# Performance work log

Measured on AMD Instinct MI355X. Metric: run time of the kernel, lower is better.

The kernel has to match this reference:

```python
import jax, jax.numpy as jnp
import numpy as np

N_EMBD = 1024
N_HEAD = 16
HEAD_SIZE = N_EMBD // N_HEAD  # 64


def setup_inputs() -> dict:
    key = jax.random.key(0)
    k1, k2, k3, k4 = jax.random.split(key, 4)
    B, T = 4, 4096
    x = jax.random.normal(k1, (B, T, N_EMBD), dtype=jnp.float32)
    scale = 1.0 / np.sqrt(N_EMBD)
    # Linear(n_embd, head_size, bias=False): store as [C, H] so projection is x @ W
    Wk = jax.random.normal(k2, (N_EMBD, HEAD_SIZE), dtype=jnp.float32) * scale
    Wq = jax.random.normal(k3, (N_EMBD, HEAD_SIZE), dtype=jnp.float32) * scale
    Wv = jax.random.normal(k4, (N_EMBD, HEAD_SIZE), dtype=jnp.float32) * scale
    decay_factor = jnp.array([-0.5], dtype=jnp.float32)
    return {"x": x, "Wk": Wk, "Wq": Wq, "Wv": Wv, "decay_factor": decay_factor}


def reference(x, Wk, Wq, Wv, decay_factor):
    B, T, C = x.shape
    H = Wk.shape[1]
    k = x @ Wk  # [B,T,H]
    q = x @ Wq  # [B,T,H]
    v = x @ Wv  # [B,T,H]
    wei = jnp.einsum('bth,bsh->bts', q, k) * (H ** -0.5)  # [B,T,T]
    idx = jnp.arange(T)
    dist = jnp.minimum(idx[None, :] - idx[:, None], 0)  # j - i, clamped max=0
    ripple_bias = dist.astype(x.dtype) * jnp.abs(decay_factor[0])
    wei = wei + ripple_bias[None, :, :]
    causal = idx[None, :] <= idx[:, None]  # tril mask [T,T]
    wei = jnp.where(causal[None, :, :], wei, -jnp.inf)
    wei = jax.nn.softmax(wei, axis=-1)
    return jnp.einsum('bts,bsh->bth', wei, v)
```

## Files before the change

kernel.cpp:

```cpp
#include <hip/hip_runtime.h>

typedef short bf16x8 __attribute__((ext_vector_type(8)));
typedef float f32x4 __attribute__((ext_vector_type(4)));

#define TT 4096
#define CC 1024
#define HH 64
#define MTOT 16384

static __device__ __forceinline__ unsigned short f2bf(float f) {
  unsigned int u = __float_as_uint(f);
  unsigned int r = (u + 0x7FFFu + ((u >> 16) & 1u)) >> 16;
  return (unsigned short)r;
}

static __device__ __forceinline__ unsigned int pack_bf2(float lo, float hi) {
  unsigned int ul = __float_as_uint(lo) + 0x8000u;
  unsigned int uh = __float_as_uint(hi) + 0x8000u;
  return __builtin_amdgcn_perm(uh, ul, 0x07060302u);
}

typedef const __attribute__((address_space(1))) void gvoid;
typedef __attribute__((address_space(3))) void svoid;
static __device__ __forceinline__ void gll16(const void* g, void* l) {
  __builtin_amdgcn_global_load_lds((gvoid*)g, (svoid*)l, 16, 0, 0);
}

#define WAITVM(N) asm volatile("s_waitcnt vmcnt(" #N ")" ::: "memory")

__global__ void prep_wt(const float* __restrict__ Wk, const float* __restrict__ Wq,
                        const float* __restrict__ Wv, unsigned short* __restrict__ Wt) {
  int r = blockIdx.x;
  const float* src = (r < 64) ? Wk : ((r < 128) ? Wq : Wv);
  int c = r & 63;
  for (int kk = threadIdx.x; kk < CC; kk += blockDim.x)
    Wt[(size_t)r * CC + kk] = f2bf(src[(size_t)kk * HH + c]);
}

__global__ __launch_bounds__(512, 2) void proj_kernel(
    const float* __restrict__ x, const unsigned short* __restrict__ Wt,
    unsigned short* __restrict__ kb, unsigned short* __restrict__ qb,
    unsigned short* __restrict__ vt) {
  extern __shared__ __align__(16) char smem[];
  float* Xl = (float*)smem;
  unsigned short* Bl = (unsigned short*)(smem + 32768);

  const int tid = threadIdx.x;
  const int lane = tid & 63;
  const int w = tid >> 6;
  const int r = lane & 15, g = lane >> 4;
  const int rowgrp = w >> 1;
  const int colbase = (w & 1) * 96;
  const int m0 = blockIdx.x * 64;

  const float* xsrcs[2];
#pragma unroll
  for (int j = 0; j < 2; ++j) {
    int c = j * 512 + tid;
    int row = c >> 4, s = c & 15;
    xsrcs[j] = x + (size_t)(m0 + row) * CC + (((s & 8) | ((s & 7) ^ (row & 7))) * 4);
  }
  const unsigned short* bsrcs[3];
#pragma unroll
  for (int j = 0; j < 3; ++j) {
    int cb = j * 512 + tid;
    int row = cb >> 3, s = cb & 7;
    bsrcs[j] = Wt + (size_t)row * CC + ((s ^ (row & 7)) * 8);
  }

  f32x4 acc[6];
#pragma unroll
  for (int n = 0; n < 6; ++n) { f32x4 z = {0.f, 0.f, 0.f, 0.f}; acc[n] = z; }

  auto stage = [&](int t, int buf) {
    float* xb = Xl + buf * 4096;
    unsigned short* bb = Bl + buf * 12288;
#pragma unroll
    for (int j = 0; j < 2; ++j)
      gll16(xsrcs[j] + t * 64, xb + (j * 512 + w * 64) * 4);
#pragma unroll
    for (int j = 0; j < 3; ++j)
      gll16(bsrcs[j] + t * 64, bb + (size_t)(j * 512 + w * 64) * 8);
  };

  const int rr = rowgrp * 16 + r;
  const int rb = rr * 64;
  const int rx = rr & 7;

  auto body = [&](int buf) {
    const float* xb = Xl + buf * 4096;
    const unsigned short* bb = Bl + buf * 12288;
    bf16x8 bfr[2][6];
#pragma unroll
    for (int ks = 0; ks < 2; ++ks)
#pragma unroll
      for (int n = 0; n < 6; ++n) {
        int col = colbase + 16 * n + r;
        bfr[ks][n] = *(const bf16x8*)&bb[col * 64 + (((ks * 4 + g) ^ (col & 7)) * 8)];
      }
#pragma unroll
    for (int ks = 0; ks < 2; ++ks) {
      int s0 = ks * 8 + 2 * g;
      f32x4 v0 = *(const f32x4*)&xb[rb + (((s0 & 8) | ((s0 & 7) ^ rx)) * 4)];
      f32x4 v1 = *(const f32x4*)&xb[rb + ((((s0 + 1) & 8) | (((s0 + 1) & 7) ^ rx)) * 4)];
      union { bf16x8 v; unsigned int u[4]; } af;
      af.u[0] = pack_bf2(v0.x, v0.y);
      af.u[1] = pack_bf2(v0.z, v0.w);
      af.u[2] = pack_bf2(v1.x, v1.y);
      af.u[3] = pack_bf2(v1.z, v1.w);
#pragma unroll
      for (int n = 0; n < 6; ++n)
        acc[n] = __builtin_amdgcn_mfma_f32_16x16x32_bf16(af.v, bfr[ks][n], acc[n], 0, 0, 0);
    }
  };

  stage(0, 0);
  stage(1, 1);

  for (int t = 0; t < 14; ++t) {
    WAITVM(5);
    __builtin_amdgcn_s_barrier();
    body(t & 1);
    __builtin_amdgcn_s_barrier();
    stage(t + 2, t & 1);
  }
  WAITVM(5); __builtin_amdgcn_s_barrier(); body(0);
  WAITVM(0); __builtin_amdgcn_s_barrier(); body(1);

#pragma unroll
  for (int n = 0; n < 6; ++n) {
#pragma unroll
    for (int i = 0; i < 4; ++i) {
      int row = m0 + rowgrp * 16 + 4 * g + i;
      int col = colbase + 16 * n + r;
      unsigned short h = f2bf(acc[n][i]);
      if (col < 64) {
        kb[(size_t)row * HH + col] = h;
      } else if (col < 128) {
        qb[(size_t)row * HH + (col - 64)] = h;
      } else {
        int dim = col - 128;
        int b = row >> 12;
        int tt = row & (TT - 1);
        vt[(((size_t)b * HH + dim) << 12) + tt] = h;
      }
    }
  }
}

__global__ __launch_bounds__(256, 2) void attn_kernel(
    const unsigned short* __restrict__ qb, const unsigned short* __restrict__ kb,
    const unsigned short* __restrict__ vt, const float* __restrict__ decayp,
    float* __restrict__ out) {
  __shared__ __align__(16) unsigned short Kl[2 * 64 * 64];
  __shared__ __align__(16) unsigned short Vl[2 * 64 * 64];
  __shared__ __align__(16) unsigned short Pl[4][16 * 64];
  __shared__ float Ml[32], Ll[32];
  __shared__ float Ol[32][64];

  const int tid = threadIdx.x;
  const int lane = tid & 63;
  const int w = tid >> 6;
  const int r = lane & 15, g = lane >> 4;
  const int qh = w & 1;
  const int kvg = w >> 1;

  const int batch = blockIdx.x & 3;
  const int qt = blockIdx.x >> 2;
  const int qbase = qt * 32;
  const int qw = qbase + qh * 16;

  const float decay = fabsf(decayp[0]);

  const unsigned short* qbb = qb + (size_t)batch * TT * HH;
  const unsigned short* kbb = kb + (size_t)batch * TT * HH;
  const unsigned short* vbb = vt + (size_t)batch * HH * TT;

  const unsigned short* qp = qbb + (size_t)(qw + r) * HH;
  bf16x8 aq0 = *(const bf16x8*)(qp + 8 * g);
  bf16x8 aq1 = *(const bf16x8*)(qp + 32 + 8 * g);

  int t0 = 0;
  if (decay > 1e-8f) {
    float wf = 60.f / decay;
    if (wf < (float)TT) {
      int W = (int)wf + 1;
      int lo = qbase - W;
      if (lo < 0) lo = 0;
      t0 = lo >> 6;
    }
  }
  const int t1 = (qbase + 31) >> 6;
  const int nsteps = (t1 - t0 + 2) >> 1;

  float m[4], lsum[4];
  f32x4 o[4];
#pragma unroll
  for (int i = 0; i < 4; ++i) {
    m[i] = -1e30f; lsum[i] = 0.f;
    f32x4 z = {0.f, 0.f, 0.f, 0.f}; o[i] = z;
  }

  for (int s = 0; s < nsteps; ++s) {
    const int tA = t0 + 2 * s;
    const int tB = (tA + 1 <= t1) ? tA + 1 : t1;
#pragma unroll
    for (int j = 0; j < 4; ++j) {
      int c = j * 256 + tid;
      int th = c >> 9;
      int cc = c & 511;
      int row = cc >> 3, sl = cc & 7;
      int tile = th ? tB : tA;
      bf16x8 kvv = *(const bf16x8*)(kbb + (size_t)(tile * 64 + row) * HH + ((sl ^ (row & 7)) * 8));
      *(bf16x8*)&Kl[c * 8] = kvv;
      bf16x8 vvv = *(const bf16x8*)(vbb + (size_t)row * TT + tile * 64 + ((sl ^ (row & 7)) * 8));
      *(bf16x8*)&Vl[c * 8] = vvv;
    }
    __syncthreads();

    const int myt = tA + kvg;
    if (myt <= t1) {
      const unsigned short* Kb = &Kl[kvg * 4096];
      const unsigned short* Vb = &Vl[kvg * 4096];
      const int kv0 = myt * 64;

      f32x4 sacc[4];
#pragma unroll
      for (int t = 0; t < 4; ++t) {
        f32x4 z = {0.f, 0.f, 0.f, 0.f}; sacc[t] = z;
        int kvr = 16 * t + r;
        bf16x8 b0 = *(const bf16x8*)&Kb[kvr * 64 + ((g ^ (kvr & 7)) * 8)];
        bf16x8 b1 = *(const bf16x8*)&Kb[kvr * 64 + (((4 + g) ^ (kvr & 7)) * 8)];
        sacc[t] = __builtin_amdgcn_mfma_f32_16x16x32_bf16(aq0, b0, sacc[t], 0, 0, 0);
        sacc[t] = __builtin_amdgcn_mfma_f32_16x16x32_bf16(aq1, b1, sacc[t], 0, 0, 0);
      }

      float p[4][4];
      float rmax[4], rsum[4], al[4];
#pragma unroll
      for (int i = 0; i < 4; ++i) rmax[i] = -1e30f;
#pragma unroll
      for (int t = 0; t < 4; ++t) {
        int kv = kv0 + 16 * t + r;
#pragma unroll
        for (int i = 0; i < 4; ++i) {
          int q = qw + 4 * g + i;
          float sv = sacc[t][i] * 0.125f + decay * (float)(kv - q);
          if (kv > q) sv = -1e30f;
          p[t][i] = sv;
          rmax[i] = fmaxf(rmax[i], sv);
        }
      }
#pragma unroll
      for (int i = 0; i < 4; ++i) {
#pragma unroll
        for (int d = 1; d < 16; d <<= 1)
          rmax[i] = fmaxf(rmax[i], __shfl_xor(rmax[i], d, 64));
        float mn = fmaxf(m[i], rmax[i]);
        al[i] = __expf(m[i] - mn);
        m[i] = mn;
        rsum[i] = 0.f;
      }
#pragma unroll
      for (int t = 0; t < 4; ++t)
#pragma unroll
        for (int i = 0; i < 4; ++i) {
          float e = __expf(p[t][i] - m[i]);
          p[t][i] = e;
          rsum[i] += e;
        }
#pragma unroll
      for (int i = 0; i < 4; ++i) {
#pragma unroll
        for (int d = 1; d < 16; d <<= 1)
          rsum[i] += __shfl_xor(rsum[i], d, 64);
        lsum[i] = lsum[i] * al[i] + rsum[i];
      }
#pragma unroll
      for (int n = 0; n < 4; ++n) {
        o[n][0] *= al[0]; o[n][1] *= al[1]; o[n][2] *= al[2]; o[n][3] *= al[3];
      }

      unsigned short* P = &Pl[w][0];
#pragma unroll
      for (int t = 0; t < 4; ++t) {
#pragma unroll
        for (int i = 0; i < 4; ++i) {
          int row = 4 * g + i;
          int col = 16 * t + r;
          int slot = col >> 3;
          P[row * 64 + ((slot ^ (row & 7)) * 8) + (col & 7)] = f2bf(p[t][i]);
        }
      }
      bf16x8 pa0 = *(const bf16x8*)&P[r * 64 + ((g ^ (r & 7)) * 8)];
      bf16x8 pa1 = *(const bf16x8*)&P[r * 64 + (((4 + g) ^ (r & 7)) * 8)];

#pragma unroll
      for (int n = 0; n < 4; ++n) {
        int dim = 16 * n + r;
        bf16x8 v0 = *(const bf16x8*)&Vb[dim * 64 + ((g ^ (dim & 7)) * 8)];
        bf16x8 v1 = *(const bf16x8*)&Vb[dim * 64 + (((4 + g) ^ (dim & 7)) * 8)];
        o[n] = __builtin_amdgcn_mfma_f32_16x16x32_bf16(pa0, v0, o[n], 0, 0, 0);
        o[n] = __builtin_amdgcn_mfma_f32_16x16x32_bf16(pa1, v1, o[n], 0, 0, 0);
      }
    }
    __syncthreads();
  }

  if (kvg == 1) {
    if (r == 0) {
#pragma unroll
      for (int i = 0; i < 4; ++i) {
        Ml[qh * 16 + 4 * g + i] = m[i];
        Ll[qh * 16 + 4 * g + i] = lsum[i];
      }
    }
#pragma unroll
    for (int n = 0; n < 4; ++n)
#pragma unroll
      for (int i = 0; i < 4; ++i)
        Ol[qh * 16 + 4 * g + i][16 * n + r] = o[n][i];
  }
  __syncthreads();
  if (kvg == 0) {
    float* ob = out + (size_t)batch * TT * HH;
#pragma unroll
    for (int i = 0; i < 4; ++i) {
      int row = qh * 16 + 4 * g + i;
      float m2 = Ml[row], l2 = Ll[row];
      float M = fmaxf(m[i], m2);
      float e1 = __expf(m[i] - M), e2 = __expf(m2 - M);
      float inv = 1.f / (lsum[i] * e1 + l2 * e2);
#pragma unroll
      for (int n = 0; n < 4; ++n) {
        float ov = (o[n][i] * e1 + Ol[row][16 * n + r] * e2) * inv;
        ob[(size_t)(qbase + row) * HH + 16 * n + r] = ov;
      }
    }
  }
}

extern "C" void kernel_launch(void* const* d_in, const int* in_sizes, int n_in,
                              void* d_out, int out_size, void* d_ws, size_t ws_size,
                              hipStream_t stream) {
  const float* x = (const float*)d_in[0];
  const float* Wk = (const float*)d_in[1];
  const float* Wq = (const float*)d_in[2];
  const float* Wv = (const float*)d_in[3];
  const float* decay = (const float*)d_in[4];
  float* out = (float*)d_out;

  unsigned short* kb = (unsigned short*)d_ws;
  unsigned short* qbw = kb + (size_t)MTOT * HH;
  unsigned short* vt = qbw + (size_t)MTOT * HH;
  unsigned short* Wt = vt + (size_t)MTOT * HH;

  prep_wt<<<dim3(192), dim3(256), 0, stream>>>(Wk, Wq, Wv, Wt);
  proj_kernel<<<dim3(256), dim3(512), 80 * 1024, stream>>>(x, Wt, kb, qbw, vt);
  attn_kernel<<<dim3(512), dim3(256), 0, stream>>>(qbw, kb, vt, decay, out);
}
```

Before: 34.52 us.

## Pipeline attention KV loads via async LDS, triple-buffer projection, transpose weights via LDS

Weight prep now transposes 64x64 tiles through shared memory with coalesced vector loads and stores, replacing strided scalar reads. The projection kernel moves from double to triple buffering with deeper vmcnt waits, which needs 120KB of LDS. The attention kernel switches to double-buffered async global-to-LDS loads that overlap with compute. It also swaps MFMA operands so each lane owns one query row, which removes most shuffles and yields coalesced float4 output stores through LDS. The larger LDS footprint may cut occupancy, and the stage/wait counts need careful bookkeeping.

```diff
diff --git a/kernel.cpp b/kernel.cpp
--- a/kernel.cpp
+++ b/kernel.cpp
@@ -30,11 +30,30 @@
 
 __global__ void prep_wt(const float* __restrict__ Wk, const float* __restrict__ Wq,
                         const float* __restrict__ Wv, unsigned short* __restrict__ Wt) {
-  int r = blockIdx.x;
-  const float* src = (r < 64) ? Wk : ((r < 128) ? Wq : Wv);
-  int c = r & 63;
-  for (int kk = threadIdx.x; kk < CC; kk += blockDim.x)
-    Wt[(size_t)r * CC + kk] = f2bf(src[(size_t)kk * HH + c]);
+  __shared__ float T[64][65];
+  const int mat = blockIdx.x >> 4;
+  const int kt = blockIdx.x & 15;
+  const float* src = (mat == 0) ? Wk : ((mat == 1) ? Wq : Wv);
+#pragma unroll
+  for (int i = 0; i < 4; ++i) {
+    int c = i * 256 + threadIdx.x;
+    int row = c >> 4, col = (c & 15) * 4;
+    f32x4 v = *(const f32x4*)&src[(size_t)(kt * 64 + row) * HH + col];
+    T[col + 0][row] = v[0];
+    T[col + 1][row] = v[1];
+    T[col + 2][row] = v[2];
+    T[col + 3][row] = v[3];
+  }
+  __syncthreads();
+#pragma unroll
+  for (int i = 0; i < 2; ++i) {
+    int c2 = i * 256 + threadIdx.x;
+    int row = c2 >> 3, k0 = (c2 & 7) * 8;
+    union { bf16x8 v; unsigned short h[8]; } pk;
+#pragma unroll
+    for (int j = 0; j < 8; ++j) pk.h[j] = f2bf(T[row][k0 + j]);
+    *(bf16x8*)&Wt[(size_t)(mat * 64 + row) * CC + kt * 64 + k0] = pk.v;
+  }
 }
 
 __global__ __launch_bounds__(512, 2) void proj_kernel(
@@ -43,7 +62,7 @@
     unsigned short* __restrict__ vt) {
   extern __shared__ __align__(16) char smem[];
   float* Xl = (float*)smem;
-  unsigned short* Bl = (unsigned short*)(smem + 32768);
+  unsigned short* Bl = (unsigned short*)(smem + 49152);
 
   const int tid = threadIdx.x;
   const int lane = tid & 63;
@@ -116,16 +135,20 @@
 
   stage(0, 0);
   stage(1, 1);
-
-  for (int t = 0; t < 14; ++t) {
-    WAITVM(5);
+  stage(2, 2);
+
+  int buf = 0;
+  for (int t = 0; t < 13; ++t) {
+    WAITVM(10);
     __builtin_amdgcn_s_barrier();
-    body(t & 1);
+    body(buf);
     __builtin_amdgcn_s_barrier();
-    stage(t + 2, t & 1);
-  }
-  WAITVM(5); __builtin_amdgcn_s_barrier(); body(0);
-  WAITVM(0); __builtin_amdgcn_s_barrier(); body(1);
+    stage(t + 3, buf);
+    buf = (buf == 2) ? 0 : buf + 1;
+  }
+  WAITVM(10); __builtin_amdgcn_s_barrier(); body(1);
+  WAITVM(5);  __builtin_amdgcn_s_barrier(); body(2);
+  WAITVM(0);  __builtin_amdgcn_s_barrier(); body(0);
 
 #pragma unroll
   for (int n = 0; n < 6; ++n) {
@@ -152,11 +175,13 @@
     const unsigned short* __restrict__ qb, const unsigned short* __restrict__ kb,
     const unsigned short* __restrict__ vt, const float* __restrict__ decayp,
     float* __restrict__ out) {
-  __shared__ __align__(16) unsigned short Kl[2 * 64 * 64];
-  __shared__ __align__(16) unsigned short Vl[2 * 64 * 64];
-  __shared__ __align__(16) unsigned short Pl[4][16 * 64];
-  __shared__ float Ml[32], Ll[32];
-  __shared__ float Ol[32][64];
+  extern __shared__ __align__(16) char smem[];
+  unsigned short* Kl = (unsigned short*)smem;
+  unsigned short* Vl = Kl + 16384;
+  unsigned short* Pl = Vl + 16384;
+  float* Ol = (float*)(smem + 65536);
+  float* Ml = (float*)(smem + 65536 + 8704);
+  float* Ll = Ml + 32;
 
   const int tid = threadIdx.x;
   const int lane = tid & 63;
@@ -169,6 +194,7 @@
   const int qt = blockIdx.x >> 2;
   const int qbase = qt * 32;
   const int qw = qbase + qh * 16;
+  const int qrow = qw + r;
 
   const float decay = fabsf(decayp[0]);
 
@@ -176,7 +202,7 @@
   const unsigned short* kbb = kb + (size_t)batch * TT * HH;
   const unsigned short* vbb = vt + (size_t)batch * HH * TT;
 
-  const unsigned short* qp = qbb + (size_t)(qw + r) * HH;
+  const unsigned short* qp = qbb + (size_t)qrow * HH;
   bf16x8 aq0 = *(const bf16x8*)(qp + 8 * g);
   bf16x8 aq1 = *(const bf16x8*)(qp + 32 + 8 * g);
 
@@ -193,150 +219,148 @@
   const int t1 = (qbase + 31) >> 6;
   const int nsteps = (t1 - t0 + 2) >> 1;
 
-  float m[4], lsum[4];
+  const unsigned short* ksrc[4];
+  const unsigned short* vsrc[4];
+#pragma unroll
+  for (int j = 0; j < 4; ++j) {
+    int c = j * 256 + tid;
+    int th = c >> 9;
+    int cc = c & 511;
+    int row = cc >> 3, sl = cc & 7;
+    ksrc[j] = kbb + (size_t)((t0 + th) * 64 + row) * HH + ((sl ^ (row & 7)) * 8);
+    vsrc[j] = vbb + (size_t)row * TT + (t0 + th) * 64 + ((sl ^ (row & 7)) * 8);
+  }
+
+  auto stage = [&](int s, int buf) {
+#pragma unroll
+    for (int j = 0; j < 4; ++j) {
+      gll16(ksrc[j] + (size_t)s * 8192, Kl + buf * 8192 + (j * 256 + w * 64) * 8);
+      gll16(vsrc[j] + s * 128, Vl + buf * 8192 + (j * 256 + w * 64) * 8);
+    }
+  };
+
+  float m = -1e30f, lsum = 0.f;
   f32x4 o[4];
 #pragma unroll
-  for (int i = 0; i < 4; ++i) {
-    m[i] = -1e30f; lsum[i] = 0.f;
-    f32x4 z = {0.f, 0.f, 0.f, 0.f}; o[i] = z;
-  }
+  for (int n = 0; n < 4; ++n) { f32x4 z = {0.f, 0.f, 0.f, 0.f}; o[n] = z; }
+
+  stage(0, 0);
 
   for (int s = 0; s < nsteps; ++s) {
-    const int tA = t0 + 2 * s;
-    const int tB = (tA + 1 <= t1) ? tA + 1 : t1;
-#pragma unroll
-    for (int j = 0; j < 4; ++j) {
-      int c = j * 256 + tid;
-      int th = c >> 9;
-      int cc = c & 511;
-      int row = cc >> 3, sl = cc & 7;
-      int tile = th ? tB : tA;
-      bf16x8 kvv = *(const bf16x8*)(kbb + (size_t)(tile * 64 + row) * HH + ((sl ^ (row & 7)) * 8));
-      *(bf16x8*)&Kl[c * 8] = kvv;
-      bf16x8 vvv = *(const bf16x8*)(vbb + (size_t)row * TT + tile * 64 + ((sl ^ (row & 7)) * 8));
-      *(bf16x8*)&Vl[c * 8] = vvv;
-    }
-    __syncthreads();
-
-    const int myt = tA + kvg;
+    if (s + 1 < nsteps) { stage(s + 1, (s + 1) & 1); WAITVM(8); }
+    else { WAITVM(0); }
+    __builtin_amdgcn_s_barrier();
+
+    const int myt = t0 + 2 * s + kvg;
     if (myt <= t1) {
-      const unsigned short* Kb = &Kl[kvg * 4096];
-      const unsigned short* Vb = &Vl[kvg * 4096];
+      const unsigned short* Kb = Kl + (s & 1) * 8192 + kvg * 4096;
+      const unsigned short* Vb = Vl + (s & 1) * 8192 + kvg * 4096;
       const int kv0 = myt * 64;
 
       f32x4 sacc[4];
+      __builtin_amdgcn_s_setprio(1);
 #pragma unroll
       for (int t = 0; t < 4; ++t) {
-        f32x4 z = {0.f, 0.f, 0.f, 0.f}; sacc[t] = z;
+        f32x4 z = {0.f, 0.f, 0.f, 0.f};
         int kvr = 16 * t + r;
         bf16x8 b0 = *(const bf16x8*)&Kb[kvr * 64 + ((g ^ (kvr & 7)) * 8)];
         bf16x8 b1 = *(const bf16x8*)&Kb[kvr * 64 + (((4 + g) ^ (kvr & 7)) * 8)];
-        sacc[t] = __builtin_amdgcn_mfma_f32_16x16x32_bf16(aq0, b0, sacc[t], 0, 0, 0);
-        sacc[t] = __builtin_amdgcn_mfma_f32_16x16x32_bf16(aq1, b1, sacc[t], 0, 0, 0);
-      }
+        z = __builtin_amdgcn_mfma_f32_16x16x32_bf16(b0, aq0, z, 0, 0, 0);
+        sacc[t] = __builtin_amdgcn_mfma_f32_16x16x32_bf16(b1, aq1, z, 0, 0, 0);
+      }
+      __builtin_amdgcn_s_setprio(0);
 
       float p[4][4];
-      float rmax[4], rsum[4], al[4];
-#pragma unroll
-      for (int i = 0; i < 4; ++i) rmax[i] = -1e30f;
+      float rmax = -1e30f;
+#pragma unroll
+      for (int t = 0; t < 4; ++t)
+#pragma unroll
+        for (int i = 0; i < 4; ++i) {
+          int kv = kv0 + 16 * t + 4 * g + i;
+          float sv = sacc[t][i] * 0.125f + decay * (float)(kv - qrow);
+          if (kv > qrow) sv = -1e30f;
+          p[t][i] = sv;
+          rmax = fmaxf(rmax, sv);
+        }
+      rmax = fmaxf(rmax, __shfl_xor(rmax, 16));
+      rmax = fmaxf(rmax, __shfl_xor(rmax, 32));
+      float mn = fmaxf(m, rmax);
+      float al = __expf(m - mn);
+      m = mn;
+      float rs = 0.f;
+#pragma unroll
+      for (int t = 0; t < 4; ++t)
+#pragma unroll
+        for (int i = 0; i < 4; ++i) {
+          float e = __expf(p[t][i] - mn);
+          p[t][i] = e;
+          rs += e;
+        }
+      rs += __shfl_xor(rs, 16);
+      rs += __shfl_xor(rs, 32);
+      lsum = lsum * al + rs;
+#pragma unroll
+      for (int n = 0; n < 4; ++n) {
+        o[n][0] *= al; o[n][1] *= al; o[n][2] *= al; o[n][3] *= al;
+      }
+
+      char* P = (char*)(Pl + w * 1024) + r * 128;
 #pragma unroll
       for (int t = 0; t < 4; ++t) {
-        int kv = kv0 + 16 * t + r;
-#pragma unroll
-        for (int i = 0; i < 4; ++i) {
-          int q = qw + 4 * g + i;
-          float sv = sacc[t][i] * 0.125f + decay * (float)(kv - q);
-          if (kv > q) sv = -1e30f;
-          p[t][i] = sv;
-          rmax[i] = fmaxf(rmax[i], sv);
-        }
-      }
-#pragma unroll
-      for (int i = 0; i < 4; ++i) {
-#pragma unroll
-        for (int d = 1; d < 16; d <<= 1)
-          rmax[i] = fmaxf(rmax[i], __shfl_xor(rmax[i], d, 64));
-        float mn = fmaxf(m[i], rmax[i]);
-        al[i] = __expf(m[i] - mn);
-        m[i] = mn;
-        rsum[i] = 0.f;
-      }
-#pragma unroll
-      for (int t = 0; t < 4; ++t)
-#pragma unroll
-        for (int i = 0; i < 4; ++i) {
-          float e = __expf(p[t][i] - m[i]);
-          p[t][i] = e;
-          rsum[i] += e;
-        }
-#pragma unroll
-      for (int i = 0; i < 4; ++i) {
-#pragma unroll
-        for (int d = 1; d < 16; d <<= 1)
-          rsum[i] += __shfl_xor(rsum[i], d, 64);
-        lsum[i] = lsum[i] * al[i] + rsum[i];
-      }
-#pragma unroll
-      for (int n = 0; n < 4; ++n) {
-        o[n][0] *= al[0]; o[n][1] *= al[1]; o[n][2] *= al[2]; o[n][3] *= al[3];
-      }
-
-      unsigned short* P = &Pl[w][0];
-#pragma unroll
-      for (int t = 0; t < 4; ++t) {
-#pragma unroll
-        for (int i = 0; i < 4; ++i) {
-          int row = 4 * g + i;
-          int col = 16 * t + r;
-          int slot = col >> 3;
-          P[row * 64 + ((slot ^ (row & 7)) * 8) + (col & 7)] = f2bf(p[t][i]);
-        }
-      }
-      bf16x8 pa0 = *(const bf16x8*)&P[r * 64 + ((g ^ (r & 7)) * 8)];
-      bf16x8 pa1 = *(const bf16x8*)&P[r * 64 + (((4 + g) ^ (r & 7)) * 8)];
-
+        uint2 u;
+        u.x = pack_bf2(p[t][0], p[t][1]);
+        u.y = pack_bf2(p[t][2], p[t][3]);
+        *(uint2*)(P + ((t ^ (r & 3)) * 32) + g * 8) = u;
+      }
+      bf16x8 pb0 = *(const bf16x8*)(P + (((g >> 1) ^ (r & 3)) * 32) + (g & 1) * 16);
+      bf16x8 pb1 = *(const bf16x8*)(P + ((((g >> 1) + 2) ^ (r & 3)) * 32) + (g & 1) * 16);
+
+      __builtin_amdgcn_s_setprio(1);
 #pragma unroll
       for (int n = 0; n < 4; ++n) {
         int dim = 16 * n + r;
         bf16x8 v0 = *(const bf16x8*)&Vb[dim * 64 + ((g ^ (dim & 7)) * 8)];
         bf16x8 v1 = *(const bf16x8*)&Vb[dim * 64 + (((4 + g) ^ (dim & 7)) * 8)];
-        o[n] = __builtin_amdgcn_mfma_f32_16x16x32_bf16(pa0, v0, o[n], 0, 0, 0);
-        o[n] = __builtin_amdgcn_mfma_f32_16x16x32_bf16(pa1, v1, o[n], 0, 0, 0);
-      }
-    }
-    __syncthreads();
-  }
-
+        o[n] = __builtin_amdgcn_mfma_f32_16x16x32_bf16(v0, pb0, o[n], 0, 0, 0);
+        o[n] = __builtin_amdgcn_mfma_f32_16x16x32_bf16(v1, pb1, o[n], 0, 0, 0);
+      }
+      __builtin_amdgcn_s_setprio(0);
+    }
+    __builtin_amdgcn_s_barrier();
+  }
+
+  const int orow = qh * 16 + r;
   if (kvg == 1) {
-    if (r == 0) {
-#pragma unroll
-      for (int i = 0; i < 4; ++i) {
-        Ml[qh * 16 + 4 * g + i] = m[i];
-        Ll[qh * 16 + 4 * g + i] = lsum[i];
-      }
-    }
+    if (lane < 16) { Ml[orow] = m; Ll[orow] = lsum; }
 #pragma unroll
     for (int n = 0; n < 4; ++n)
 #pragma unroll
       for (int i = 0; i < 4; ++i)
-        Ol[qh * 16 + 4 * g + i][16 * n + r] = o[n][i];
+        Ol[orow * 68 + 16 * n + 4 * g + i] = o[n][i];
   }
   __syncthreads();
   if (kvg == 0) {
-    float* ob = out + (size_t)batch * TT * HH;
-#pragma unroll
-    for (int i = 0; i < 4; ++i) {
-      int row = qh * 16 + 4 * g + i;
-      float m2 = Ml[row], l2 = Ll[row];
-      float M = fmaxf(m[i], m2);
-      float e1 = __expf(m[i] - M), e2 = __expf(m2 - M);
-      float inv = 1.f / (lsum[i] * e1 + l2 * e2);
-#pragma unroll
-      for (int n = 0; n < 4; ++n) {
-        float ov = (o[n][i] * e1 + Ol[row][16 * n + r] * e2) * inv;
-        ob[(size_t)(qbase + row) * HH + 16 * n + r] = ov;
-      }
-    }
+    float m2 = Ml[orow], l2 = Ll[orow];
+    float M = fmaxf(m, m2);
+    float e1 = __expf(m - M), e2 = __expf(m2 - M);
+    float inv = 1.f / (lsum * e1 + l2 * e2);
+#pragma unroll
+    for (int n = 0; n < 4; ++n)
+#pragma unroll
+      for (int i = 0; i < 4; ++i) {
+        int d = 16 * n + 4 * g + i;
+        Ol[orow * 68 + d] = (o[n][i] * e1 + Ol[orow * 68 + d] * e2) * inv;
+      }
+  }
+  __syncthreads();
+
+  float* ob = out + (size_t)batch * TT * HH;
+#pragma unroll
+  for (int j = 0; j < 2; ++j) {
+    int c = j * 256 + tid;
+    int row = c >> 4, q4 = (c & 15) * 4;
+    f32x4 vv = *(const f32x4*)&Ol[row * 68 + q4];
+    *(f32x4*)&ob[(size_t)(qbase + row) * HH + q4] = vv;
   }
 }
 
@@ -355,7 +379,7 @@
   unsigned short* vt = qbw + (size_t)MTOT * HH;
   unsigned short* Wt = vt + (size_t)MTOT * HH;
 
-  prep_wt<<<dim3(192), dim3(256), 0, stream>>>(Wk, Wq, Wv, Wt);
-  proj_kernel<<<dim3(256), dim3(512), 80 * 1024, stream>>>(x, Wt, kb, qbw, vt);
-  attn_kernel<<<dim3(512), dim3(256), 0, stream>>>(qbw, kb, vt, decay, out);
-}
+  prep_wt<<<dim3(48), dim3(256), 0, stream>>>(Wk, Wq, Wv, Wt);
+  proj_kernel<<<dim3(256), dim3(512), 120 * 1024, stream>>>(x, Wt, kb, qbw, vt);
+  attn_kernel<<<dim3(512), dim3(256), 74496, stream>>>(qbw, kb, vt, decay, out);
+}
```

New measurement: 33.49 us. 1.03x faster.
